# Optimization experiments

Hardware: AMD Instinct MI355X
Metric: run time of the kernel (lower is better)

Reference implementation:

```python
import jax, jax.numpy as jnp
import numpy as np

TEMPERATURE = 0.1
NUM_CLASSES = 32
BATCH = 8192
HIDDEN = 256


def setup_inputs() -> dict:
    key = jax.random.key(0)
    k1, k2 = jax.random.split(key)
    features = jax.random.normal(k1, (BATCH, HIDDEN), dtype=jnp.float32)
    labels = jax.random.randint(k2, (BATCH,), 0, NUM_CLASSES)
    return {"features": features, "labels": labels}


def reference(features, labels):
    B = features.shape[0]
    # L2 normalize rows, pairwise cosine sim scaled by temperature
    f = features / jnp.linalg.norm(features, axis=1, keepdims=True)
    sim = (f @ f.T) / TEMPERATURE                       # [B, B]
    offdiag = 1.0 - jnp.eye(B, dtype=sim.dtype)
    E = jnp.exp(sim) * offdiag                          # exp sims, self excluded

    onehot = (labels[:, None] == jnp.arange(NUM_CLASSES)[None, :]).astype(sim.dtype)  # [B, C]
    # per-anchor, per-class sum of exp-sims (excluding self)
    class_sum = E @ onehot                              # [B, C]
    # per-anchor class counts excluding self
    counts = onehot.sum(0)[None, :] - onehot            # [B, C]
    # denominator_i = sum over classes with members (excluding i) of class mean
    denom = jnp.where(counts > 0, class_sum / jnp.maximum(counts, 1.0), 0.0).sum(axis=1)  # [B]

    # positives: same label, not self
    pos_mask = (onehot @ onehot.T) * offdiag            # [B, B]
    P = pos_mask.sum(axis=1)                            # number of positives per anchor
    valid = P > 0
    # -mean_p log(exp(sim[i,p]) / denom_i) = log(denom_i) - mean_p sim[i,p]
    mean_pos_sim = (sim * pos_mask).sum(axis=1) / jnp.maximum(P, 1.0)
    loss_i = jnp.where(valid, jnp.log(jnp.maximum(denom, 1e-30)) - mean_pos_sim, 0.0)

    n_valid = valid.sum()
    loss = jnp.where(n_valid > 0, loss_i.sum() / jnp.maximum(n_valid, 1).astype(sim.dtype), 0.0)
    return loss
```

## Files before the change

### kernel.cpp

```cpp
#include <hip/hip_runtime.h>
#include <hip/hip_bf16.h>
#include <math.h>
#include <string.h>

#define B_SZ  8192
#define KD    256
#define NCLS  32
#define NCHUNK 8
#define JTPC   8
#define SCALE_LOG2 3.79828243f
#define LN2 0.69314718056f

typedef __attribute__((ext_vector_type(8))) short short8;
typedef __attribute__((ext_vector_type(4))) float f32x4;

static __device__ __forceinline__ unsigned pk2bf(float a, float b) {
    __hip_bfloat162 h = __float22bfloat162_rn(make_float2(a, b));
    unsigned u; __builtin_memcpy(&u, &h, 4); return u;
}
static __device__ __forceinline__ float fexp2(float x) {
    float r;
    asm("v_exp_f32 %0, %1" : "=v"(r) : "v"(x));
    return r;
}

__global__ void prep_kernel(const float* __restrict__ feat, unsigned short* __restrict__ Fbf) {
    int row  = blockIdx.x * 4 + (threadIdx.x >> 6);
    int lane = threadIdx.x & 63;
    const float4 v = ((const float4*)(feat + (size_t)row * KD))[lane];
    float s = v.x * v.x + v.y * v.y + v.z * v.z + v.w * v.w;
    #pragma unroll
    for (int off = 1; off < 64; off <<= 1) s += __shfl_xor(s, off, 64);
    float rn = rsqrtf(s) * SCALE_LOG2;
    uint2 w;
    w.x = pk2bf(v.x * rn, v.y * rn);
    w.y = pk2bf(v.z * rn, v.w * rn);
    ((uint2*)(Fbf + (size_t)row * KD))[lane] = w;
}

__global__ void count_kernel(const int* __restrict__ labels, int* __restrict__ counts) {
    __shared__ int sc[NCLS];
    int t = threadIdx.x;
    if (t < NCLS) sc[t] = 0;
    __syncthreads();
    for (int i = t; i < B_SZ; i += 256) atomicAdd(&sc[labels[i]], 1);
    __syncthreads();
    if (t < NCLS) counts[t] = sc[t];
}

__global__ __launch_bounds__(256, 2) void sim_kernel(
    const unsigned short* __restrict__ Fbf, const int* __restrict__ labels,
    float* __restrict__ pcls, float* __restrict__ ppos)
{
    __shared__ __align__(16) unsigned short sbuf[2][2][128 * 64];
    __shared__ int   slab[2][128];
    __shared__ float sps[128];

    const int bid = blockIdx.x;
    const int swz = (bid & 7) * 64 + (bid >> 3);
    const int itile = swz >> 3;
    const int jc    = swz & 7;
    const int i0    = itile * 128;

    const int t    = threadIdx.x;
    const int wave = t >> 6;
    const int lane = t & 63;
    const int wr   = wave >> 1;
    const int wc   = wave & 1;
    const int l15  = lane & 15;
    const int l4   = lane >> 4;

    int labi[4];
    #pragma unroll
    for (int m = 0; m < 4; m++) labi[m] = labels[i0 + wr * 64 + m * 16 + l15];

    const int rT = t >> 3;
    const int s8 = t & 7;

    auto STAGE = [&](int buf, int j0s, int ks) {
        const int kc = ks * 64;
        #pragma unroll
        for (int a = 0; a < 4; ++a) {
            int r   = a * 32 + rT;
            int sl  = s8 ^ (r & 7);
            int col = kc + sl * 8;
            const unsigned short* gA = Fbf + (size_t)(i0 + r) * KD + col;
            char* lA = (char*)&sbuf[buf][0][0] + a * 4096 + wave * 1024;
            __builtin_amdgcn_global_load_lds(
                (const __attribute__((address_space(1))) void*)gA,
                (__attribute__((address_space(3))) void*)lA, 16, 0, 0);
            const unsigned short* gB = Fbf + (size_t)(j0s + r) * KD + col;
            char* lB = (char*)&sbuf[buf][1][0] + a * 4096 + wave * 1024;
            __builtin_amdgcn_global_load_lds(
                (const __attribute__((address_space(1))) void*)gB,
                (__attribute__((address_space(3))) void*)lB, 16, 0, 0);
        }
    };

    f32x4 acc_cs[4][2];
    float psum[4] = {0.f, 0.f, 0.f, 0.f};
    #pragma unroll
    for (int m = 0; m < 4; m++)
        #pragma unroll
        for (int cb = 0; cb < 2; cb++)
            acc_cs[m][cb] = (f32x4){0.f, 0.f, 0.f, 0.f};

    const int jt_beg = jc * JTPC, jt_end = (jc + 1) * JTPC;
    if (t < 128) slab[0][t] = labels[jt_beg * 128 + t];
    STAGE(0, jt_beg * 128, 0);

    #pragma unroll 1
    for (int jt = jt_beg; jt < jt_end; ++jt) {
        const int j0 = jt * 128;
        const int cur = jt & 1;

        __syncthreads();

        f32x4 acc[4][4];
        #pragma unroll
        for (int m = 0; m < 4; m++)
            #pragma unroll
            for (int n = 0; n < 4; n++)
                acc[m][n] = (f32x4){0.f, 0.f, 0.f, 0.f};

        #pragma unroll 1
        for (int ks = 0; ks < 4; ++ks) {
            if (ks < 3) STAGE((ks + 1) & 1, j0, ks + 1);
            const unsigned short* pA = &sbuf[ks & 1][0][0];
            const unsigned short* pB = &sbuf[ks & 1][1][0];
            short8 bf4[4][2];
            #pragma unroll
            for (int n = 0; n < 4; ++n) {
                int r = wc * 64 + n * 16 + l15;
                #pragma unroll
                for (int kk = 0; kk < 2; ++kk)
                    bf4[n][kk] = *(const short8*)&pB[r * 64 + (((kk * 4 + l4) ^ (r & 7)) * 8)];
            }
            __builtin_amdgcn_s_setprio(1);
            #pragma unroll
            for (int m = 0; m < 4; ++m) {
                int r = wr * 64 + m * 16 + l15;
                short8 a0 = *(const short8*)&pA[r * 64 + ((l4 ^ (r & 7)) * 8)];
                short8 a1 = *(const short8*)&pA[r * 64 + (((4 + l4) ^ (r & 7)) * 8)];
                #pragma unroll
                for (int n = 0; n < 4; ++n) {
                    acc[m][n] = __builtin_amdgcn_mfma_f32_16x16x32_bf16(bf4[n][0], a0, acc[m][n], 0, 0, 0);
                    acc[m][n] = __builtin_amdgcn_mfma_f32_16x16x32_bf16(bf4[n][1], a1, acc[m][n], 0, 0, 0);
                }
            }
            __builtin_amdgcn_s_setprio(0);
            __syncthreads();
        }

        if (jt + 1 < jt_end) STAGE(0, (jt + 1) * 128, 0);
        if (jt + 1 < jt_end && t < 128) slab[cur ^ 1][t] = labels[(jt + 1) * 128 + t];

        char* sEw = (char*)&sbuf[1][0][0] + wave * 8192;

        int4 lj4[4];
        #pragma unroll
        for (int n = 0; n < 4; n++)
            lj4[n] = *(const int4*)&slab[cur][wc * 64 + n * 16 + l4 * 4];

        if (j0 != i0) {
            #pragma unroll
            for (int m = 0; m < 4; m++) {
                const int row = m * 16 + l15;
                #pragma unroll
                for (int n = 0; n < 4; n++) {
                    const int* ljp = (const int*)&lj4[n];
                    float e[4];
                    #pragma unroll
                    for (int q = 0; q < 4; q++) {
                        float sp = acc[m][n][q];
                        psum[m] += (ljp[q] == labi[m]) ? sp : 0.0f;
                        e[q] = fexp2(sp);
                    }
                    uint2 w; w.x = pk2bf(e[0], e[1]); w.y = pk2bf(e[2], e[3]);
                    const int bc = (n * 32 + l4 * 8) ^ ((row & 7) << 4);
                    *(uint2*)(sEw + row * 128 + bc) = w;
                }
            }
        } else {
            #pragma unroll
            for (int m = 0; m < 4; m++) {
                const int row = m * 16 + l15;
                const int ig = i0 + wr * 64 + row;
                #pragma unroll
                for (int n = 0; n < 4; n++) {
                    const int jb = wc * 64 + n * 16 + l4 * 4;
                    const int* ljp = (const int*)&lj4[n];
                    float e[4];
                    #pragma unroll
                    for (int q = 0; q < 4; q++) {
                        const int jg = j0 + jb + q;
                        float sp = acc[m][n][q];
                        bool self = (ig == jg);
                        psum[m] += (!self && ljp[q] == labi[m]) ? sp : 0.0f;
                        e[q] = self ? 0.0f : fexp2(sp);
                    }
                    uint2 w; w.x = pk2bf(e[0], e[1]); w.y = pk2bf(e[2], e[3]);
                    const int bc = (n * 32 + l4 * 8) ^ ((row & 7) << 4);
                    *(uint2*)(sEw + row * 128 + bc) = w;
                }
            }
        }

        short8 hf[2][2];
        #pragma unroll
        for (int kk = 0; kk < 2; kk++) {
            const int jb = wc * 64 + kk * 32 + l4 * 8;
            int4 lv0 = *(const int4*)&slab[cur][jb];
            int4 lv1 = *(const int4*)&slab[cur][jb + 4];
            int lv[8] = {lv0.x, lv0.y, lv0.z, lv0.w, lv1.x, lv1.y, lv1.z, lv1.w};
            #pragma unroll
            for (int cb = 0; cb < 2; cb++) {
                short8 h;
                #pragma unroll
                for (int e = 0; e < 8; e++)
                    h[e] = (lv[e] == cb * 16 + l15) ? (short)0x3F80 : (short)0;
                hf[kk][cb] = h;
            }
        }

        #pragma unroll
        for (int kk = 0; kk < 2; kk++) {
            #pragma unroll
            for (int m = 0; m < 4; m++) {
                const int row = m * 16 + l15;
                const int bc = (kk * 64 + l4 * 16) ^ ((row & 7) << 4);
                short8 ef = *(const short8*)(sEw + row * 128 + bc);
                #pragma unroll
                for (int cb = 0; cb < 2; cb++)
                    acc_cs[m][cb] = __builtin_amdgcn_mfma_f32_16x16x32_bf16(
                        ef, hf[kk][cb], acc_cs[m][cb], 0, 0, 0);
            }
        }
    }

    __syncthreads();
    float* scr = (float*)&sbuf[0][0][0];
    float pv[4];
    #pragma unroll
    for (int m = 0; m < 4; m++) {
        float v = psum[m];
        v += __shfl_xor(v, 16, 64);
        v += __shfl_xor(v, 32, 64);
        pv[m] = v;
    }
    if (wc == 1) {
        #pragma unroll
        for (int m = 0; m < 4; m++) {
            #pragma unroll
            for (int cb = 0; cb < 2; cb++)
                #pragma unroll
                for (int q = 0; q < 4; q++)
                    scr[(wr * 64 + m * 16 + l4 * 4 + q) * 33 + cb * 16 + l15] =
                        acc_cs[m][cb][q];
            if (l4 == 0) sps[wr * 64 + m * 16 + l15] = pv[m];
        }
    }
    __syncthreads();
    if (wc == 0) {
        const size_t slot = (size_t)itile * NCHUNK + jc;
        float* pc = pcls + slot * 128 * NCLS;
        #pragma unroll
        for (int m = 0; m < 4; m++) {
            #pragma unroll
            for (int cb = 0; cb < 2; cb++)
                #pragma unroll
                for (int q = 0; q < 4; q++) {
                    const int r = wr * 64 + m * 16 + l4 * 4 + q;
                    const int c = cb * 16 + l15;
                    pc[r * NCLS + c] = acc_cs[m][cb][q] + scr[r * 33 + c];
                }
            if (l4 == 0)
                ppos[slot * 128 + wr * 64 + m * 16 + l15] =
                    (pv[m] + sps[wr * 64 + m * 16 + l15]) * LN2;
        }
    }
}

__global__ void reduce_kernel(const float* __restrict__ pcls, const float* __restrict__ ppos,
                              const int* __restrict__ counts, const int* __restrict__ labels,
                              float* __restrict__ loss_i, float* __restrict__ validf) {
    int tid = blockIdx.x * blockDim.x + threadIdx.x;
    int i  = tid >> 3;
    int cq = tid & 7;
    if (i >= B_SZ) return;
    int itile = i >> 7, ilocal = i & 127;

    f32x4 cs = (f32x4){0.f, 0.f, 0.f, 0.f};
    for (int ch = 0; ch < NCHUNK; ch++) {
        const float* p = pcls + ((size_t)(itile * NCHUNK + ch) * 128 + ilocal) * NCLS + cq * 4;
        f32x4 v = *(const f32x4*)p;
        cs = cs + v;
    }
    int labi = labels[i];
    float dpart = 0.0f;
    #pragma unroll
    for (int e = 0; e < 4; e++) {
        int c = cq * 4 + e;
        int cnt = counts[c] - (c == labi ? 1 : 0);
        if (cnt > 0) dpart += cs[e] / (float)cnt;
    }
    #pragma unroll
    for (int off = 1; off < 8; off <<= 1) dpart += __shfl_xor(dpart, off, 64);

    if (cq == 0) {
        float psum = 0.0f;
        for (int ch = 0; ch < NCHUNK; ch++)
            psum += ppos[(size_t)(itile * NCHUNK + ch) * 128 + ilocal];
        int P = counts[labi] - 1;
        bool valid = P > 0;
        float li = 0.0f;
        if (valid) li = logf(fmaxf(dpart, 1e-30f)) - psum / (float)max(P, 1);
        loss_i[i] = li;
        validf[i] = valid ? 1.0f : 0.0f;
    }
}

__global__ void final_kernel(const float* __restrict__ loss_i, const float* __restrict__ validf,
                             float* __restrict__ out) {
    __shared__ float ssum[256];
    __shared__ float scnt[256];
    int t = threadIdx.x;
    float s = 0.0f, c = 0.0f;
    for (int i = t; i < B_SZ; i += 256) { s += loss_i[i]; c += validf[i]; }
    ssum[t] = s; scnt[t] = c;
    __syncthreads();
    #pragma unroll
    for (int off = 128; off > 0; off >>= 1) {
        if (t < off) { ssum[t] += ssum[t + off]; scnt[t] += scnt[t + off]; }
        __syncthreads();
    }
    if (t == 0) out[0] = (scnt[0] > 0.0f) ? ssum[0] / scnt[0] : 0.0f;
}

extern "C" void kernel_launch(void* const* d_in, const int* in_sizes, int n_in,
                              void* d_out, int out_size, void* d_ws, size_t ws_size,
                              hipStream_t stream) {
    const float* feat   = (const float*)d_in[0];
    const int*   labels = (const int*)d_in[1];
    float*       out    = (float*)d_out;

    char* ws = (char*)d_ws;
    size_t off = 0;
    auto alloc = [&](size_t bytes) -> void* {
        void* p = ws + off;
        off = (off + bytes + 255) & ~(size_t)255;
        return p;
    };

    unsigned short* Fbf = (unsigned short*)alloc((size_t)B_SZ * KD * 2);
    int*   counts = (int*)alloc((size_t)NCLS * 4);
    float* loss_i = (float*)alloc((size_t)B_SZ * 4);
    float* validf = (float*)alloc((size_t)B_SZ * 4);
    float* ppos   = (float*)alloc((size_t)512 * 128 * 4);
    float* pcls   = (float*)alloc((size_t)512 * 128 * NCLS * 4);

    prep_kernel<<<B_SZ / 4, 256, 0, stream>>>(feat, Fbf);
    count_kernel<<<1, 256, 0, stream>>>(labels, counts);
    sim_kernel<<<512, 256, 0, stream>>>(Fbf, labels, pcls, ppos);
    reduce_kernel<<<B_SZ * 8 / 256, 256, 0, stream>>>(pcls, ppos, counts, labels, loss_i, validf);
    final_kernel<<<1, 256, 0, stream>>>(loss_i, validf, out);
}
```

Measured before the change: 83.65 us.

## Store per-class partials as bf16 and rotate j-tile order per block

Partial per-class exp-sum buffers are written in bf16 instead of fp32, which halves the store traffic from the sim kernel and the load traffic in the reduce kernel. The order in which each block walks its eight j-tiles is also rotated by block index, so blocks sharing a chunk do not all read the same B tile at the same moment. The bf16 rounding of partial sums adds error to the loss.

```diff
diff --git a/kernel.cpp b/kernel.cpp
--- a/kernel.cpp
+++ b/kernel.cpp
@@ -18,6 +18,10 @@
     __hip_bfloat162 h = __float22bfloat162_rn(make_float2(a, b));
     unsigned u; __builtin_memcpy(&u, &h, 4); return u;
 }
+static __device__ __forceinline__ unsigned short f2bf1(float f) {
+    unsigned u = __float_as_uint(f);
+    return (unsigned short)((u + 0x7FFF + ((u >> 16) & 1)) >> 16);
+}
 static __device__ __forceinline__ float fexp2(float x) {
     float r;
     asm("v_exp_f32 %0, %1" : "=v"(r) : "v"(x));
@@ -50,7 +54,7 @@
 
 __global__ __launch_bounds__(256, 2) void sim_kernel(
     const unsigned short* __restrict__ Fbf, const int* __restrict__ labels,
-    float* __restrict__ pcls, float* __restrict__ ppos)
+    unsigned short* __restrict__ pcls, float* __restrict__ ppos)
 {
     __shared__ __align__(16) unsigned short sbuf[2][2][128 * 64];
     __shared__ int   slab[2][128];
@@ -105,14 +109,19 @@
         for (int cb = 0; cb < 2; cb++)
             acc_cs[m][cb] = (f32x4){0.f, 0.f, 0.f, 0.f};
 
-    const int jt_beg = jc * JTPC, jt_end = (jc + 1) * JTPC;
-    if (t < 128) slab[0][t] = labels[jt_beg * 128 + t];
-    STAGE(0, jt_beg * 128, 0);
+    const int jt_beg = jc * JTPC;
+    const int rot = bid & 7;
+    {
+        const int jf0 = (jt_beg + rot) * 128;
+        if (t < 128) slab[0][t] = labels[jf0 + t];
+        STAGE(0, jf0, 0);
+    }
 
     #pragma unroll 1
-    for (int jt = jt_beg; jt < jt_end; ++jt) {
+    for (int k = 0; k < JTPC; ++k) {
+        const int jt = jt_beg + ((k + rot) & 7);
         const int j0 = jt * 128;
-        const int cur = jt & 1;
+        const int cur = k & 1;
 
         __syncthreads();
 
@@ -152,8 +161,11 @@
             __syncthreads();
         }
 
-        if (jt + 1 < jt_end) STAGE(0, (jt + 1) * 128, 0);
-        if (jt + 1 < jt_end && t < 128) slab[cur ^ 1][t] = labels[(jt + 1) * 128 + t];
+        if (k + 1 < JTPC) {
+            const int jn0 = (jt_beg + ((k + 1 + rot) & 7)) * 128;
+            STAGE(0, jn0, 0);
+            if (t < 128) slab[cur ^ 1][t] = labels[jn0 + t];
+        }
 
         char* sEw = (char*)&sbuf[1][0][0] + wave * 8192;
 
@@ -263,7 +275,7 @@
     __syncthreads();
     if (wc == 0) {
         const size_t slot = (size_t)itile * NCHUNK + jc;
-        float* pc = pcls + slot * 128 * NCLS;
+        unsigned short* pc = pcls + slot * 128 * NCLS;
         #pragma unroll
         for (int m = 0; m < 4; m++) {
             #pragma unroll
@@ -272,7 +284,7 @@
                 for (int q = 0; q < 4; q++) {
                     const int r = wr * 64 + m * 16 + l4 * 4 + q;
                     const int c = cb * 16 + l15;
-                    pc[r * NCLS + c] = acc_cs[m][cb][q] + scr[r * 33 + c];
+                    pc[r * NCLS + c] = f2bf1(acc_cs[m][cb][q] + scr[r * 33 + c]);
                 }
             if (l4 == 0)
                 ppos[slot * 128 + wr * 64 + m * 16 + l15] =
@@ -281,7 +293,7 @@
     }
 }
 
-__global__ void reduce_kernel(const float* __restrict__ pcls, const float* __restrict__ ppos,
+__global__ void reduce_kernel(const unsigned short* __restrict__ pcls, const float* __restrict__ ppos,
                               const int* __restrict__ counts, const int* __restrict__ labels,
                               float* __restrict__ loss_i, float* __restrict__ validf) {
     int tid = blockIdx.x * blockDim.x + threadIdx.x;
@@ -292,9 +304,12 @@
 
     f32x4 cs = (f32x4){0.f, 0.f, 0.f, 0.f};
     for (int ch = 0; ch < NCHUNK; ch++) {
-        const float* p = pcls + ((size_t)(itile * NCHUNK + ch) * 128 + ilocal) * NCLS + cq * 4;
-        f32x4 v = *(const f32x4*)p;
-        cs = cs + v;
+        const unsigned short* p = pcls + ((size_t)(itile * NCHUNK + ch) * 128 + ilocal) * NCLS + cq * 4;
+        ushort4 v = *(const ushort4*)p;
+        const unsigned short* vp = (const unsigned short*)&v;
+        #pragma unroll
+        for (int e = 0; e < 4; e++)
+            cs[e] += __uint_as_float((unsigned)vp[e] << 16);
     }
     int labi = labels[i];
     float dpart = 0.0f;
@@ -357,7 +372,7 @@
     float* loss_i = (float*)alloc((size_t)B_SZ * 4);
     float* validf = (float*)alloc((size_t)B_SZ * 4);
     float* ppos   = (float*)alloc((size_t)512 * 128 * 4);
-    float* pcls   = (float*)alloc((size_t)512 * 128 * NCLS * 4);
+    unsigned short* pcls = (unsigned short*)alloc((size_t)512 * 128 * NCLS * 2);
 
     prep_kernel<<<B_SZ / 4, 256, 0, stream>>>(feat, Fbf);
     count_kernel<<<1, 256, 0, stream>>>(labels, counts);
```

New measurement: 85.01 us. Within noise of the previous version (+1.6%).

## Fuse label counting into prep and final reduction into reduce kernel

Applied to the files above, without the earlier changes.

Label counting moves into the first 32 blocks of the normalization kernel, with per-block shared histograms merged into global counts by atomics. The final mean reduction is folded into the reduce kernel through block reductions, fixed-point integer atomics and a last-block ticket. This drops two kernel launches and the loss_i/validf round trip, but adds a memset, and the fixed-point accumulation at scale 2048 introduces rounding error and overflow risk in the loss sum.

```diff
diff --git a/kernel.cpp b/kernel.cpp
--- a/kernel.cpp
+++ b/kernel.cpp
@@ -10,6 +10,7 @@
 #define JTPC   8
 #define SCALE_LOG2 3.79828243f
 #define LN2 0.69314718056f
+#define ACC_SCALE 2048.0f
 
 typedef __attribute__((ext_vector_type(8))) short short8;
 typedef __attribute__((ext_vector_type(4))) float f32x4;
@@ -24,9 +25,20 @@
     return r;
 }
 
-__global__ void prep_kernel(const float* __restrict__ feat, unsigned short* __restrict__ Fbf) {
-    int row  = blockIdx.x * 4 + (threadIdx.x >> 6);
-    int lane = threadIdx.x & 63;
+__global__ void prep_kernel(const float* __restrict__ feat, unsigned short* __restrict__ Fbf,
+                            const int* __restrict__ labels, int* __restrict__ counts) {
+    __shared__ int sc[NCLS];
+    const int blk = blockIdx.x;
+    const int t   = threadIdx.x;
+    const bool docnt = (blk < 32);
+    if (docnt) {
+        if (t < NCLS) sc[t] = 0;
+        __syncthreads();
+        atomicAdd(&sc[labels[blk * 256 + t]], 1);
+    }
+
+    int row  = blk * 4 + (t >> 6);
+    int lane = t & 63;
     const float4 v = ((const float4*)(feat + (size_t)row * KD))[lane];
     float s = v.x * v.x + v.y * v.y + v.z * v.z + v.w * v.w;
     #pragma unroll
@@ -36,16 +48,11 @@
     w.x = pk2bf(v.x * rn, v.y * rn);
     w.y = pk2bf(v.z * rn, v.w * rn);
     ((uint2*)(Fbf + (size_t)row * KD))[lane] = w;
-}
-
-__global__ void count_kernel(const int* __restrict__ labels, int* __restrict__ counts) {
-    __shared__ int sc[NCLS];
-    int t = threadIdx.x;
-    if (t < NCLS) sc[t] = 0;
-    __syncthreads();
-    for (int i = t; i < B_SZ; i += 256) atomicAdd(&sc[labels[i]], 1);
-    __syncthreads();
-    if (t < NCLS) counts[t] = sc[t];
+
+    if (docnt) {
+        __syncthreads();
+        if (t < NCLS) atomicAdd(&counts[t], sc[t]);
+    }
 }
 
 __global__ __launch_bounds__(256, 2) void sim_kernel(
@@ -283,11 +290,13 @@
 
 __global__ void reduce_kernel(const float* __restrict__ pcls, const float* __restrict__ ppos,
                               const int* __restrict__ counts, const int* __restrict__ labels,
-                              float* __restrict__ loss_i, float* __restrict__ validf) {
+                              int* __restrict__ acc_loss, int* __restrict__ acc_valid,
+                              int* __restrict__ ticket, float* __restrict__ out) {
+    __shared__ float ssum[256];
+    __shared__ float scnt[256];
     int tid = blockIdx.x * blockDim.x + threadIdx.x;
     int i  = tid >> 3;
     int cq = tid & 7;
-    if (i >= B_SZ) return;
     int itile = i >> 7, ilocal = i & 127;
 
     f32x4 cs = (f32x4){0.f, 0.f, 0.f, 0.f};
@@ -307,34 +316,36 @@
     #pragma unroll
     for (int off = 1; off < 8; off <<= 1) dpart += __shfl_xor(dpart, off, 64);
 
+    float li = 0.0f, vf = 0.0f;
     if (cq == 0) {
         float psum = 0.0f;
         for (int ch = 0; ch < NCHUNK; ch++)
             psum += ppos[(size_t)(itile * NCHUNK + ch) * 128 + ilocal];
         int P = counts[labi] - 1;
-        bool valid = P > 0;
-        float li = 0.0f;
-        if (valid) li = logf(fmaxf(dpart, 1e-30f)) - psum / (float)max(P, 1);
-        loss_i[i] = li;
-        validf[i] = valid ? 1.0f : 0.0f;
-    }
-}
-
-__global__ void final_kernel(const float* __restrict__ loss_i, const float* __restrict__ validf,
-                             float* __restrict__ out) {
-    __shared__ float ssum[256];
-    __shared__ float scnt[256];
+        if (P > 0) {
+            li = logf(fmaxf(dpart, 1e-30f)) - psum / (float)P;
+            vf = 1.0f;
+        }
+    }
     int t = threadIdx.x;
-    float s = 0.0f, c = 0.0f;
-    for (int i = t; i < B_SZ; i += 256) { s += loss_i[i]; c += validf[i]; }
-    ssum[t] = s; scnt[t] = c;
+    ssum[t] = li; scnt[t] = vf;
     __syncthreads();
     #pragma unroll
     for (int off = 128; off > 0; off >>= 1) {
         if (t < off) { ssum[t] += ssum[t + off]; scnt[t] += scnt[t + off]; }
         __syncthreads();
     }
-    if (t == 0) out[0] = (scnt[0] > 0.0f) ? ssum[0] / scnt[0] : 0.0f;
+    if (t == 0) {
+        atomicAdd(acc_loss, __float2int_rn(ssum[0] * ACC_SCALE));
+        atomicAdd(acc_valid, (int)(scnt[0] + 0.5f));
+        __threadfence();
+        int tk = atomicAdd(ticket, 1);
+        if (tk == 255) {
+            int ls = atomicAdd(acc_loss, 0);
+            int nv = atomicAdd(acc_valid, 0);
+            out[0] = (nv > 0) ? ((float)ls / ACC_SCALE) / (float)nv : 0.0f;
+        }
+    }
 }
 
 extern "C" void kernel_launch(void* const* d_in, const int* in_sizes, int n_in,
@@ -352,16 +363,19 @@
         return p;
     };
 
+    int* ctrl = (int*)alloc(256);
+    int* counts    = ctrl;
+    int* acc_loss  = ctrl + 32;
+    int* acc_valid = ctrl + 33;
+    int* ticket    = ctrl + 34;
+
     unsigned short* Fbf = (unsigned short*)alloc((size_t)B_SZ * KD * 2);
-    int*   counts = (int*)alloc((size_t)NCLS * 4);
-    float* loss_i = (float*)alloc((size_t)B_SZ * 4);
-    float* validf = (float*)alloc((size_t)B_SZ * 4);
     float* ppos   = (float*)alloc((size_t)512 * 128 * 4);
     float* pcls   = (float*)alloc((size_t)512 * 128 * NCLS * 4);
 
-    prep_kernel<<<B_SZ / 4, 256, 0, stream>>>(feat, Fbf);
-    count_kernel<<<1, 256, 0, stream>>>(labels, counts);
+    hipMemsetAsync(ctrl, 0, 256, stream);
+    prep_kernel<<<B_SZ / 4, 256, 0, stream>>>(feat, Fbf, labels, counts);
     sim_kernel<<<512, 256, 0, stream>>>(Fbf, labels, pcls, ppos);
-    reduce_kernel<<<B_SZ * 8 / 256, 256, 0, stream>>>(pcls, ppos, counts, labels, loss_i, validf);
-    final_kernel<<<1, 256, 0, stream>>>(loss_i, validf, out);
-}
+    reduce_kernel<<<B_SZ * 8 / 256, 256, 0, stream>>>(pcls, ppos, counts, labels,
+                                                      acc_loss, acc_valid, ticket, out);
+}
```

After: 80.26 us (median of 2 runs). 1.04x faster.
